# Optimization experiments

Measured on AMD Instinct MI355X. Metric: run time of the kernel, lower is better.

The kernel has to match this reference:

```python
import math
import jax, jax.numpy as jnp
import numpy as np

B, S, D, H = 4, 2048, 1024, 16
HD = D // H
SAMPLING_FACTOR = 5.0


def setup_inputs() -> dict:
    key = jax.random.key(0)
    ks = jax.random.split(key, 6)
    std = 1.0 / math.sqrt(D)
    inp = {
        "x": jax.random.normal(ks[0], (B, S, D), dtype=jnp.float32),
        "Wq": jax.random.normal(ks[1], (D, D), dtype=jnp.float32) * std,
        "bq": jnp.zeros((D,), dtype=jnp.float32),
        "Wk": jax.random.normal(ks[2], (D, D), dtype=jnp.float32) * std,
        "bk": jnp.zeros((D,), dtype=jnp.float32),
        "Wv": jax.random.normal(ks[3], (D, D), dtype=jnp.float32) * std,
        "bv": jnp.zeros((D,), dtype=jnp.float32),
        "Wo": jax.random.normal(ks[4], (D, D), dtype=jnp.float32) * std,
        "bo": jnp.zeros((D,), dtype=jnp.float32),
        "sample_idx": jax.random.randint(ks[5], (S,), 0, S, dtype=jnp.int32),
    }
    return inp


def reference(x, Wq, bq, Wk, bk, Wv, bv, Wo, bo, sample_idx):
    batch, seq_len, d_model = x.shape
    scale = math.sqrt(HD)
    # u = number of top (active) queries; U_part = seq_len here (sampling saturates)
    u = max(1, min(seq_len, int(SAMPLING_FACTOR * math.log(seq_len + 1))))

    def proj(W, b):
        # [B,S,D] -> [B,H,S,hd]
        return (x @ W + b).reshape(batch, seq_len, H, HD).transpose(0, 2, 1, 3)

    Q = proj(Wq, bq)
    K = proj(Wk, bk)
    V = proj(Wv, bv)

    # sparsity measure over sampled keys (with replacement)
    K_sample = K[:, :, sample_idx, :]                     # [B,H,U,hd]
    scores_sample = jnp.einsum("bhsd,bhud->bhsu", Q, K_sample) / scale
    M = scores_sample.max(axis=-1) - scores_sample.mean(axis=-1)  # [B,H,S]

    _, top_idx = jax.lax.top_k(M, u)                      # [B,H,u]

    Q_reduce = jnp.take_along_axis(Q, top_idx[..., None], axis=2)  # [B,H,u,hd]
    attn_scores = jnp.einsum("bhud,bhsd->bhus", Q_reduce, K) / scale
    attn_probs = jax.nn.softmax(attn_scores, axis=-1)
    context = jnp.einsum("bhus,bhsd->bhud", attn_probs, V)        # [B,H,u,hd]

    # fill lazy queries with mean of V, scatter active-query contexts
    V_mean = V.mean(axis=2, keepdims=True)                # [B,H,1,hd]
    out = jnp.broadcast_to(V_mean, (batch, H, seq_len, HD))
    b_idx = jnp.arange(batch)[:, None, None]
    h_idx = jnp.arange(H)[None, :, None]
    out = out.at[b_idx, h_idx, top_idx].set(context)      # [B,H,S,hd]

    out = out.transpose(0, 2, 1, 3).reshape(batch, seq_len, d_model)
    return out @ Wo + bo
```

## Files before the change

### kernel.cpp

```cpp
#include <hip/hip_runtime.h>
#include <math.h>
#include <stdint.h>
#include <stddef.h>

#define BB 4
#define SS 2048
#define DD 1024
#define HH 16
#define HD 64
#define UU 38
#define BH (BB*HH)
#define NROWS (BB*SS)
#define QSZ (BB*HH*SS*HD)
#define NSPLIT 16
#define SPLEN (SS/NSPLIT)
#define QPAD 40

typedef unsigned short ushortT;
typedef unsigned int u32;
typedef __attribute__((ext_vector_type(8))) short bf16x8;
typedef __attribute__((ext_vector_type(4))) float f32x4;

static __device__ __forceinline__ ushortT f2bf(float f) {
  union { float f; unsigned int u; } v; v.f = f;
  unsigned int r = v.u + 0x7fffu + ((v.u >> 16) & 1u);
  return (ushortT)(r >> 16);
}
static __device__ __forceinline__ float bf2f(ushortT h) {
  union { unsigned int u; float f; } v; v.u = ((unsigned int)h) << 16; return v.f;
}
static __device__ __forceinline__ void gld16(const void* g, void* l) {
  __builtin_amdgcn_global_load_lds((const __attribute__((address_space(1))) u32*)g,
                                   (__attribute__((address_space(3))) u32*)l, 16, 0, 0);
}

__global__ __launch_bounds__(256) void split_x(
    const float* __restrict__ x, ushortT* __restrict__ xh, ushortT* __restrict__ xl)
{
  size_t i = ((size_t)blockIdx.x * 256 + threadIdx.x) * 8;
  float4 v0 = *(const float4*)&x[i];
  float4 v1 = *(const float4*)&x[i + 4];
  float fv[8] = {v0.x, v0.y, v0.z, v0.w, v1.x, v1.y, v1.z, v1.w};
  bf16x8 hv, lv;
#pragma unroll
  for (int j = 0; j < 8; ++j) {
    ushortT h = f2bf(fv[j]);
    hv[j] = (short)h;
    lv[j] = (short)f2bf(fv[j] - bf2f(h));
  }
  *(bf16x8*)&xh[i] = hv;
  *(bf16x8*)&xl[i] = lv;
}

__global__ __launch_bounds__(256) void splitT_kernel(
    const float* __restrict__ Wq, const float* __restrict__ Wk, const float* __restrict__ Wv,
    ushortT* __restrict__ WqhT, ushortT* __restrict__ WqlT,
    ushortT* __restrict__ WkhT, ushortT* __restrict__ WklT,
    ushortT* __restrict__ WvhT, ushortT* __restrict__ WvlT)
{
  __shared__ float tile[64][65];
  const int z = blockIdx.z;
  const float* W = (z == 0) ? Wq : (z == 1) ? Wk : Wv;
  ushortT* WhT = (z == 0) ? WqhT : (z == 1) ? WkhT : WvhT;
  ushortT* WlT = (z == 0) ? WqlT : (z == 1) ? WklT : WvlT;
  const int t = threadIdx.x;
  const int bk = blockIdx.y * 64, bn = blockIdx.x * 64;
  const int rr = t >> 4, c4 = (t & 15) * 4;
#pragma unroll
  for (int p = 0; p < 4; ++p) {
    int row = rr + p * 16;
    float4 v = *(const float4*)&W[(size_t)(bk + row) * DD + bn + c4];
    tile[row][c4] = v.x; tile[row][c4+1] = v.y; tile[row][c4+2] = v.z; tile[row][c4+3] = v.w;
  }
  __syncthreads();
  const int n = t & 63, ks = (t >> 6) * 16;
  union { ushortT us[16]; uint4 q[2]; } hb, lb;
#pragma unroll
  for (int j = 0; j < 16; ++j) {
    float f = tile[ks + j][n];
    ushortT h = f2bf(f);
    hb.us[j] = h;
    lb.us[j] = f2bf(f - bf2f(h));
  }
  size_t o = ((size_t)(bn + n) * DD + (size_t)(bk + ks)) >> 3;
  ((uint4*)WhT)[o] = hb.q[0]; ((uint4*)WhT)[o + 1] = hb.q[1];
  ((uint4*)WlT)[o] = lb.q[0]; ((uint4*)WlT)[o + 1] = lb.q[1];
}

__global__ __launch_bounds__(256) void dedupe_kernel(
    const int* __restrict__ sidx, int* __restrict__ uidx, int* __restrict__ ucount,
    float* __restrict__ Vsum, float* __restrict__ Ksum)
{
  __shared__ unsigned bm[64];
  __shared__ int base[64];
  const int t = threadIdx.x;
  for (int i = t; i < BH * HD; i += 256) { Vsum[i] = 0.f; Ksum[i] = 0.f; }
  if (t < 64) bm[t] = 0;
  __syncthreads();
  for (int s = t; s < SS; s += 256) {
    int v = sidx[s];
    atomicOr(&bm[v >> 5], 1u << (v & 31));
  }
  __syncthreads();
  if (t < 64) {
    int c = __popc(bm[t]);
    int pre = c;
#pragma unroll
    for (int off = 1; off < 64; off <<= 1) {
      int o = __shfl_up(pre, off, 64);
      if (t >= off) pre += o;
    }
    base[t] = pre - c;
    if (t == 63) ucount[0] = pre;
  }
  __syncthreads();
  if (t < 64) {
    unsigned m = bm[t];
    int o = base[t];
    while (m) {
      int b = __ffs(m) - 1;
      uidx[o++] = t * 32 + b;
      m &= m - 1;
    }
  }
  __syncthreads();
  int total = ucount[0];
  int padded = (total + 127) & ~127;
  int first = uidx[0];
  for (int i = total + t; i < padded; i += 256) uidx[i] = first;
}

__global__ __launch_bounds__(256, 4) void gemm_qkv(
    const ushortT* __restrict__ Axh, const ushortT* __restrict__ Axl,
    const ushortT* __restrict__ WqhT, const ushortT* __restrict__ WqlT,
    const ushortT* __restrict__ WkhT, const ushortT* __restrict__ WklT,
    const ushortT* __restrict__ WvhT, const ushortT* __restrict__ WvlT,
    const float* __restrict__ bq, const float* __restrict__ bk, const float* __restrict__ bv,
    ushortT* __restrict__ Qhg, ushortT* __restrict__ Qlg,
    ushortT* __restrict__ Khg, ushortT* __restrict__ Klg,
    float* __restrict__ V, float* __restrict__ Vsum)
{
  __shared__ ushortT As[128 * 64];
  __shared__ ushortT Bs[128 * 64];
  const int t = threadIdx.x;
  const int lin = blockIdx.x;
  const int xcd = lin & 7;
  const int idx = lin >> 3;
  const int m_loc = idx & 7;
  const int n_idx = idx >> 3;
  const int m0 = (xcd * 8 + m_loc) * 128;
  const int p = n_idx >> 3;
  const int n0 = (n_idx & 7) * 128;
  const ushortT* Bh = (p == 0) ? WqhT : (p == 1) ? WkhT : WvhT;
  const ushortT* Bl = (p == 0) ? WqlT : (p == 1) ? WklT : WvlT;
  const float* bias = (p == 0) ? bq : (p == 1) ? bk : bv;
  const int NTk = (p == 2) ? 32 : 48;
  const int lane = t & 63, w = t >> 6;
  const int wr = w >> 1, wc = w & 1;
  const int fr = lane & 15, fs = lane >> 4;
  const int srow = t >> 3, sslot = t & 7;
  f32x4 acc[4][4];
#pragma unroll
  for (int i = 0; i < 4; ++i)
#pragma unroll
    for (int j = 0; j < 4; ++j) acc[i][j] = (f32x4){0.f, 0.f, 0.f, 0.f};

  for (int kt = 0; kt < NTk; ++kt) {
    const int seg = kt >> 4;
    const int rk0 = (kt & 15) * 64;
    const ushortT* a_src = (seg == 1) ? Axl : Axh;
    const ushortT* b_src = (seg == 2) ? Bl : Bh;
    __syncthreads();
#pragma unroll
    for (int is = 0; is < 4; ++is) {
      int row = is * 32 + srow;
      int soff = ((sslot ^ (row & 7)) * 8);
      int cb = (is * 256 + (t & 192)) * 8;
      gld16(&a_src[(size_t)(m0 + row) * DD + rk0 + soff], &As[cb]);
      gld16(&b_src[(size_t)(n0 + row) * DD + rk0 + soff], &Bs[cb]);
    }
    __syncthreads();
#pragma unroll
    for (int kk = 0; kk < 2; ++kk) {
      bf16x8 af[4], bf[4];
#pragma unroll
      for (int i = 0; i < 4; ++i) {
        int row = wr * 64 + i * 16 + fr;
        af[i] = *(const bf16x8*)&As[row * 64 + (((kk * 4 + fs) ^ (row & 7)) * 8)];
      }
#pragma unroll
      for (int j = 0; j < 4; ++j) {
        int row = wc * 64 + j * 16 + fr;
        bf[j] = *(const bf16x8*)&Bs[row * 64 + (((kk * 4 + fs) ^ (row & 7)) * 8)];
      }
#pragma unroll
      for (int i = 0; i < 4; ++i)
#pragma unroll
        for (int j = 0; j < 4; ++j)
          acc[i][j] = __builtin_amdgcn_mfma_f32_16x16x32_bf16(af[i], bf[j], acc[i][j], 0, 0, 0);
    }
  }
  float csum[4] = {0.f, 0.f, 0.f, 0.f};
#pragma unroll
  for (int i = 0; i < 4; ++i) {
#pragma unroll
    for (int j = 0; j < 4; ++j) {
      int c = n0 + wc * 64 + j * 16 + fr;
      float bs = bias[c];
      int h = c >> 6, hd = c & 63;
#pragma unroll
      for (int r = 0; r < 4; ++r) {
        int m = m0 + wr * 64 + i * 16 + fs * 4 + r;
        int b = m >> 11, s = m & (SS - 1);
        size_t oidx = (((size_t)(b * HH + h)) * SS + s) * HD + hd;
        float val = acc[i][j][r] + bs;
        if (p == 2) {
          V[oidx] = val;
          csum[j] += val;
        } else {
          ushortT hv = f2bf(val);
          ushortT lv = f2bf(val - bf2f(hv));
          if (p == 0) { Qhg[oidx] = hv; Qlg[oidx] = lv; }
          else        { Khg[oidx] = hv; Klg[oidx] = lv; }
        }
      }
    }
  }
  if (p == 2) {
    __syncthreads();
    float* red = (float*)As;
    int slot = wr * 4 + fs;
#pragma unroll
    for (int j = 0; j < 4; ++j)
      red[(wc * 64 + j * 16 + fr) * 8 + slot] = csum[j];
    __syncthreads();
    if (t < 128) {
      float s = 0.f;
#pragma unroll
      for (int g = 0; g < 8; ++g) s += red[t * 8 + g];
      int c = n0 + t;
      int h = c >> 6, hd = c & 63;
      atomicAdd(&Vsum[((m0 >> 11) * HH + h) * HD + hd], s);
    }
  }
}

__global__ __launch_bounds__(256) void means_kernel(
    const ushortT* __restrict__ Khg, const ushortT* __restrict__ Klg,
    const int* __restrict__ sidx, float* __restrict__ Ksum)
{
  __shared__ float rk[4][64];
  const int bh = blockIdx.x;
  const int sp = blockIdx.y;
  const int t = threadIdx.x;
  const int d = t & 63, pq = t >> 6;
  float ka = 0.f;
  const int r0 = sp * 512 + pq * 128;
  for (int r = r0; r < r0 + 128; ++r) {
    size_t ki = ((size_t)bh * SS + sidx[r]) * HD + d;
    ka += bf2f(Khg[ki]) + bf2f(Klg[ki]);
  }
  rk[pq][d] = ka;
  __syncthreads();
  if (t < 64)
    atomicAdd(&Ksum[bh * HD + t], rk[0][t] + rk[1][t] + rk[2][t] + rk[3][t]);
}

__global__ __launch_bounds__(256, 3) void m_mfma(
    const ushortT* __restrict__ Qhg, const ushortT* __restrict__ Qlg,
    const ushortT* __restrict__ Khg, const ushortT* __restrict__ Klg,
    const int* __restrict__ uidx, const int* __restrict__ ucount,
    const float* __restrict__ Ksum, float* __restrict__ M)
{
  __shared__ ushortT KhL[128 * 64], KlL[128 * 64];
  __shared__ float Mred[2][128];
  __shared__ float km[64];
  const int t = threadIdx.x;
  const int lin = blockIdx.x;
  const int swz = (lin & 7) * 128 + (lin >> 3);
  const int bh = swz >> 4;
  const int s0 = (swz & 15) * 128;
  const int lane = t & 63, w = t >> 6;
  const int wr = w >> 1, wc = w & 1;
  const int fr = lane & 15, fs = lane >> 4;
  if (t < 64) km[t] = Ksum[bh * HD + t] * (1.0f / SS);
  const int srow = t >> 3, sslot = t & 7;
  const int ntiles = (ucount[0] + 127) >> 7;
  const size_t qbase = (size_t)bh * SS + s0;
  float runmax[4][4];
#pragma unroll
  for (int i = 0; i < 4; ++i)
#pragma unroll
    for (int r = 0; r < 4; ++r) runmax[i][r] = -INFINITY;

  for (int ui = 0; ui < ntiles; ++ui) {
    __syncthreads();
#pragma unroll
    for (int is = 0; is < 4; ++is) {
      int row = is * 32 + srow;
      int gr = uidx[ui * 128 + row];
      int soff = ((sslot ^ (row & 7)) * 8);
      int cb = (is * 256 + (t & 192)) * 8;
      size_t ga = ((size_t)bh * SS + gr) * HD + soff;
      gld16(&Khg[ga], &KhL[cb]);
      gld16(&Klg[ga], &KlL[cb]);
    }
    __syncthreads();
    f32x4 acc[4][4];
#pragma unroll
    for (int i = 0; i < 4; ++i)
#pragma unroll
      for (int j = 0; j < 4; ++j) acc[i][j] = (f32x4){0.f, 0.f, 0.f, 0.f};
#pragma unroll
    for (int kk = 0; kk < 2; ++kk) {
      bf16x8 ah[4], al[4], bh[4], bl[4];
#pragma unroll
      for (int i = 0; i < 4; ++i) {
        size_t ga = (qbase + (size_t)(wr * 64 + i * 16 + fr)) * HD + kk * 32 + fs * 8;
        ah[i] = *(const bf16x8*)&Qhg[ga];
        al[i] = *(const bf16x8*)&Qlg[ga];
      }
#pragma unroll
      for (int j = 0; j < 4; ++j) {
        int row = wc * 64 + j * 16 + fr;
        int off = row * 64 + (((kk * 4 + fs) ^ (row & 7)) * 8);
        bh[j] = *(const bf16x8*)&KhL[off];
        bl[j] = *(const bf16x8*)&KlL[off];
      }
#pragma unroll
      for (int i = 0; i < 4; ++i)
#pragma unroll
        for (int j = 0; j < 4; ++j) {
          acc[i][j] = __builtin_amdgcn_mfma_f32_16x16x32_bf16(ah[i], bh[j], acc[i][j], 0, 0, 0);
          acc[i][j] = __builtin_amdgcn_mfma_f32_16x16x32_bf16(ah[i], bl[j], acc[i][j], 0, 0, 0);
          acc[i][j] = __builtin_amdgcn_mfma_f32_16x16x32_bf16(al[i], bh[j], acc[i][j], 0, 0, 0);
        }
    }
#pragma unroll
    for (int i = 0; i < 4; ++i)
#pragma unroll
      for (int j = 0; j < 4; ++j)
#pragma unroll
        for (int r = 0; r < 4; ++r) runmax[i][r] = fmaxf(runmax[i][r], acc[i][j][r]);
  }
#pragma unroll
  for (int i = 0; i < 4; ++i)
#pragma unroll
    for (int r = 0; r < 4; ++r) {
      float v = runmax[i][r];
      v = fmaxf(v, __shfl_xor(v, 1, 64));
      v = fmaxf(v, __shfl_xor(v, 2, 64));
      v = fmaxf(v, __shfl_xor(v, 4, 64));
      v = fmaxf(v, __shfl_xor(v, 8, 64));
      runmax[i][r] = v;
    }
  if (fr == 0) {
#pragma unroll
    for (int i = 0; i < 4; ++i)
#pragma unroll
      for (int r = 0; r < 4; ++r)
        Mred[wc][wr * 64 + i * 16 + fs * 4 + r] = runmax[i][r];
  }
  __syncthreads();
  if (t < 128) {
    float mx = fmaxf(Mred[0][t], Mred[1][t]);
    float md = 0.f;
    const ushortT* qh = &Qhg[(qbase + t) * HD];
    const ushortT* ql = &Qlg[(qbase + t) * HD];
#pragma unroll
    for (int k8 = 0; k8 < 8; ++k8) {
      bf16x8 hv = *(const bf16x8*)&qh[k8 * 8];
      bf16x8 lv = *(const bf16x8*)&ql[k8 * 8];
#pragma unroll
      for (int j = 0; j < 8; ++j)
        md += (bf2f((ushortT)hv[j]) + bf2f((ushortT)lv[j])) * km[k8 * 8 + j];
    }
    M[(size_t)bh * SS + s0 + t] = (mx - md) * 0.125f;
  }
}

__global__ __launch_bounds__(256) void topk_kernel(const float* __restrict__ M,
                                                   int* __restrict__ topi)
{
  __shared__ float rw[4];
  __shared__ int   ri4[4];
  __shared__ int   winner;
  const int t = threadIdx.x, bh = blockIdx.x;
  const int lane = t & 63, w = t >> 6;
  float v[8];
#pragma unroll
  for (int j = 0; j < 8; ++j) v[j] = M[(size_t)bh * SS + t + j * 256];
  for (int it = 0; it < UU; ++it) {
    float bv = v[0]; int bj = 0;
#pragma unroll
    for (int j = 1; j < 8; ++j) if (v[j] > bv) { bv = v[j]; bj = j; }
    int bs = t + bj * 256;
#pragma unroll
    for (int off = 32; off > 0; off >>= 1) {
      float ov = __shfl_xor(bv, off, 64);
      int os = __shfl_xor(bs, off, 64);
      if (ov > bv || (ov == bv && os < bs)) { bv = ov; bs = os; }
    }
    if (lane == 0) { rw[w] = bv; ri4[w] = bs; }
    __syncthreads();
    if (t == 0) {
      float fv = rw[0]; int fsx = ri4[0];
#pragma unroll
      for (int g = 1; g < 4; ++g)
        if (rw[g] > fv || (rw[g] == fv && ri4[g] < fsx)) { fv = rw[g]; fsx = ri4[g]; }
      topi[bh * UU + it] = fsx;
      winner = fsx;
    }
    __syncthreads();
    int wi = winner;
    if ((wi & 255) == t) {
      int jj = wi >> 8;
#pragma unroll
      for (int j = 0; j < 8; ++j) if (j == jj) v[j] = -INFINITY;
    }
  }
}

__global__ __launch_bounds__(256) void attn_flash(
    const ushortT* __restrict__ Qhg, const ushortT* __restrict__ Qlg,
    const ushortT* __restrict__ Khg, const ushortT* __restrict__ Klg,
    const float* __restrict__ V, const int* __restrict__ topi,
    float* __restrict__ pacc, float* __restrict__ pm, float* __restrict__ pl)
{
  __shared__ float Qt[64][68];
  __shared__ float KV[64][68];
  __shared__ float Ps[64][68];
  __shared__ float redA[16][64];
  __shared__ float redB[16][64];
  __shared__ float mrow[64], lrow[64], scl[64];
  const int t  = threadIdx.x;
  const int bh = blockIdx.x;
  const int sp = blockIdx.y;
  const float* Vb = V + (size_t)bh * SS * HD;
  if (t < 64) { mrow[t] = -INFINITY; lrow[t] = 0.f; }
  {
    int q = t >> 2, k4 = (t & 3) * 16;
    float fv[16];
#pragma unroll
    for (int e = 0; e < 16; ++e) fv[e] = 0.f;
    if (q < UU) {
      int qidx = topi[bh * UU + q];
      size_t ga = ((size_t)bh * SS + qidx) * HD + k4;
      bf16x8 h0 = *(const bf16x8*)&Qhg[ga];
      bf16x8 h1 = *(const bf16x8*)&Qhg[ga + 8];
      bf16x8 l0 = *(const bf16x8*)&Qlg[ga];
      bf16x8 l1 = *(const bf16x8*)&Qlg[ga + 8];
#pragma unroll
      for (int j = 0; j < 8; ++j) {
        fv[j]     = bf2f((ushortT)h0[j]) + bf2f((ushortT)l0[j]);
        fv[8 + j] = bf2f((ushortT)h1[j]) + bf2f((ushortT)l1[j]);
      }
    }
#pragma unroll
    for (int e = 0; e < 16; ++e) Qt[k4 + e][q] = fv[e];
  }
  const int q4 = (t & 15) * 4, j4g = (t >> 4) * 4, d4 = (t >> 4) * 4;
  const int lj = t >> 2, lk4 = (t & 3) * 16;
  float acc[4][4] = {};
  for (int s0 = sp * SPLEN; s0 < (sp + 1) * SPLEN; s0 += 64) {
    __syncthreads();
    {
      size_t ga = ((size_t)bh * SS + s0 + lj) * HD + lk4;
      bf16x8 h0 = *(const bf16x8*)&Khg[ga];
      bf16x8 h1 = *(const bf16x8*)&Khg[ga + 8];
      bf16x8 l0 = *(const bf16x8*)&Klg[ga];
      bf16x8 l1 = *(const bf16x8*)&Klg[ga + 8];
#pragma unroll
      for (int j = 0; j < 8; ++j) {
        KV[lk4 + j][lj]     = bf2f((ushortT)h0[j]) + bf2f((ushortT)l0[j]);
        KV[lk4 + 8 + j][lj] = bf2f((ushortT)h1[j]) + bf2f((ushortT)l1[j]);
      }
    }
    __syncthreads();
    float sacc[4][4] = {};
#pragma unroll 16
    for (int k = 0; k < 64; ++k) {
      float4 a = *(const float4*)&Qt[k][q4];
      float4 b = *(const float4*)&KV[k][j4g];
      sacc[0][0] += a.x*b.x; sacc[0][1] += a.x*b.y; sacc[0][2] += a.x*b.z; sacc[0][3] += a.x*b.w;
      sacc[1][0] += a.y*b.x; sacc[1][1] += a.y*b.y; sacc[1][2] += a.y*b.z; sacc[1][3] += a.y*b.w;
      sacc[2][0] += a.z*b.x; sacc[2][1] += a.z*b.y; sacc[2][2] += a.z*b.z; sacc[2][3] += a.z*b.w;
      sacc[3][0] += a.w*b.x; sacc[3][1] += a.w*b.y; sacc[3][2] += a.w*b.z; sacc[3][3] += a.w*b.w;
    }
#pragma unroll
    for (int i = 0; i < 4; ++i) {
      float mx = fmaxf(fmaxf(sacc[i][0], sacc[i][1]), fmaxf(sacc[i][2], sacc[i][3]));
      redA[t >> 4][q4 + i] = mx;
    }
    __syncthreads();
    if (t < 64) {
      float mx = redA[0][t];
#pragma unroll
      for (int g = 1; g < 16; ++g) mx = fmaxf(mx, redA[g][t]);
      float mn = fmaxf(mrow[t], mx * 0.125f);
      scl[t] = __expf(mrow[t] - mn);
      mrow[t] = mn;
    }
    __syncthreads();
    float4 vld[4];
#pragma unroll
    for (int i = 0; i < 4; ++i)
      vld[i] = *(const float4*)&Vb[(size_t)(s0 + lj) * HD + lk4 + 4 * i];
    float psum[4] = {};
#pragma unroll
    for (int i = 0; i < 4; ++i) {
#pragma unroll
      for (int j = 0; j < 4; ++j) {
        float e = __expf(sacc[i][j] * 0.125f - mrow[q4 + i]);
        Ps[j4g + j][q4 + i] = e;
        psum[i] += e;
      }
      redB[t >> 4][q4 + i] = psum[i];
    }
#pragma unroll
    for (int i = 0; i < 4; ++i)
      *(float4*)&KV[lj][lk4 + 4 * i] = vld[i];
    __syncthreads();
    if (t < 64) {
      float ts = redB[0][t];
#pragma unroll
      for (int g = 1; g < 16; ++g) ts += redB[g][t];
      lrow[t] = lrow[t] * scl[t] + ts;
    }
#pragma unroll
    for (int i = 0; i < 4; ++i) {
      float fsc = scl[q4 + i];
      acc[i][0] *= fsc; acc[i][1] *= fsc; acc[i][2] *= fsc; acc[i][3] *= fsc;
    }
#pragma unroll 16
    for (int j = 0; j < 64; ++j) {
      float4 a = *(const float4*)&Ps[j][q4];
      float4 b = *(const float4*)&KV[j][d4];
      acc[0][0] += a.x*b.x; acc[0][1] += a.x*b.y; acc[0][2] += a.x*b.z; acc[0][3] += a.x*b.w;
      acc[1][0] += a.y*b.x; acc[1][1] += a.y*b.y; acc[1][2] += a.y*b.z; acc[1][3] += a.y*b.w;
      acc[2][0] += a.z*b.x; acc[2][1] += a.z*b.y; acc[2][2] += a.z*b.z; acc[2][3] += a.z*b.w;
      acc[3][0] += a.w*b.x; acc[3][1] += a.w*b.y; acc[3][2] += a.w*b.z; acc[3][3] += a.w*b.w;
    }
  }
  const size_t pb = ((size_t)bh * NSPLIT + sp) * QPAD;
#pragma unroll
  for (int i = 0; i < 4; ++i) {
    int q = q4 + i;
    if (q < UU) {
#pragma unroll
      for (int j = 0; j < 4; ++j)
        pacc[(pb + q) * HD + d4 + j] = acc[i][j];
    }
  }
  if (t < UU) { pm[pb + t] = mrow[t]; pl[pb + t] = lrow[t]; }
}

__global__ __launch_bounds__(256) void base_kernel(
    const float* __restrict__ Vsum, const float* __restrict__ Wo,
    const float* __restrict__ bo, float* __restrict__ base)
{
  __shared__ float red[16][BB][16];
  const int t = threadIdx.x;
  const int cl = t & 15, kg = t >> 4;
  const int c = blockIdx.x * 16 + cl;
  float acc[BB] = {};
  for (int k = kg * 64; k < kg * 64 + 64; ++k) {
    float w = Wo[(size_t)k * DD + c];
#pragma unroll
    for (int b = 0; b < BB; ++b) acc[b] += Vsum[b * DD + k] * w;
  }
#pragma unroll
  for (int b = 0; b < BB; ++b) red[kg][b][cl] = acc[b];
  __syncthreads();
  if (t < 64) {
    int b = t >> 4, cc = blockIdx.x * 16 + (t & 15);
    float s = 0.f;
#pragma unroll
    for (int g = 0; g < 16; ++g) s += red[g][b][t & 15];
    base[b * DD + cc] = s * (1.0f / SS) + bo[cc];
  }
}

__global__ void fill_kernel(const float* __restrict__ base, float* __restrict__ out)
{
  size_t i = (size_t)blockIdx.x * 256 + threadIdx.x;
  float4 bv = ((const float4*)base)[(i >> 19) * 256 + (i & 255)];
  ((float4*)out)[i] = bv;
}

__global__ __launch_bounds__(256) void scatter_kernel(
    const float* __restrict__ pacc, const float* __restrict__ pm,
    const float* __restrict__ pl, const float* __restrict__ Vsum,
    const int* __restrict__ topi, const float* __restrict__ Wo,
    float* __restrict__ out)
{
  __shared__ float delta[64];
  const int t  = threadIdx.x;
  const int bh = blockIdx.x;
  const int u  = blockIdx.y;
  const int b = bh >> 4, h = bh & 15;
  const int s = topi[bh * UU + u];
  if (t < 64) {
    float mv[NSPLIT];
    float ms = -INFINITY;
#pragma unroll
    for (int sp = 0; sp < NSPLIT; ++sp) {
      mv[sp] = pm[((size_t)bh * NSPLIT + sp) * QPAD + u];
      ms = fmaxf(ms, mv[sp]);
    }
    float l = 0.f, c = 0.f;
#pragma unroll
    for (int sp = 0; sp < NSPLIT; ++sp) {
      float wv = __expf(mv[sp] - ms);
      l += wv * pl[((size_t)bh * NSPLIT + sp) * QPAD + u];
      c += wv * pacc[(((size_t)bh * NSPLIT + sp) * QPAD + u) * HD + t];
    }
    delta[t] = c / l - Vsum[bh * HD + t] * (1.0f / SS);
  }
  __syncthreads();
  float* orow = out + ((size_t)b * SS + s) * DD;
#pragma unroll
  for (int j = 0; j < 4; ++j) {
    int c = t + j * 256;
    float acc = 0.f;
#pragma unroll 8
    for (int d = 0; d < 64; ++d) acc += delta[d] * Wo[(size_t)(h * HD + d) * DD + c];
    atomicAdd(&orow[c], acc);
  }
}

extern "C" void kernel_launch(void* const* d_in, const int* in_sizes, int n_in,
                              void* d_out, int out_size, void* d_ws, size_t ws_size,
                              hipStream_t stream) {
  const float* x  = (const float*)d_in[0];
  const float* Wq = (const float*)d_in[1];
  const float* bq = (const float*)d_in[2];
  const float* Wk = (const float*)d_in[3];
  const float* bk = (const float*)d_in[4];
  const float* Wv = (const float*)d_in[5];
  const float* bv = (const float*)d_in[6];
  const float* Wo = (const float*)d_in[7];
  const float* bo = (const float*)d_in[8];
  const int* sidx = (const int*)d_in[9];
  float* out = (float*)d_out;

  float* f     = (float*)d_ws;
  float* V     = f;
  float* Ksum  = f + (size_t)QSZ;
  float* Vsum  = Ksum + BH * HD;
  float* Mbuf  = Vsum + BH * HD;
  float* base  = Mbuf + (size_t)BH * SS;
  float* ctx   = base + BB * DD;
  float* pacc  = ctx + (size_t)BH * UU * HD;
  float* pm    = pacc + (size_t)BH * NSPLIT * QPAD * HD;
  float* pl    = pm + (size_t)BH * NSPLIT * QPAD;
  int*   topi  = (int*)(pl + (size_t)BH * NSPLIT * QPAD);
  int*   uidx  = topi + 4096;
  int*   ucount= uidx + 4096;
  ushortT* usp = (ushortT*)(ucount + 64);
  ushortT* WqhT = usp;
  ushortT* WqlT = WqhT + (size_t)DD * DD;
  ushortT* WkhT = WqlT + (size_t)DD * DD;
  ushortT* WklT = WkhT + (size_t)DD * DD;
  ushortT* WvhT = WklT + (size_t)DD * DD;
  ushortT* WvlT = WvhT + (size_t)DD * DD;
  ushortT* xh   = WvlT + (size_t)DD * DD;
  ushortT* xl   = xh + (size_t)NROWS * DD;
  ushortT* Qhg  = xl + (size_t)NROWS * DD;
  ushortT* Qlg  = Qhg + (size_t)QSZ;
  ushortT* Khg  = Qlg + (size_t)QSZ;
  ushortT* Klg  = Khg + (size_t)QSZ;

  split_x<<<NROWS * DD / (256 * 8), 256, 0, stream>>>(x, xh, xl);
  splitT_kernel<<<dim3(16, 16, 3), 256, 0, stream>>>(Wq, Wk, Wv, WqhT, WqlT,
                                                     WkhT, WklT, WvhT, WvlT);
  dedupe_kernel<<<1, 256, 0, stream>>>(sidx, uidx, ucount, Vsum, Ksum);
  gemm_qkv<<<1536, 256, 0, stream>>>(xh, xl, WqhT, WqlT, WkhT, WklT, WvhT, WvlT,
                                     bq, bk, bv, Qhg, Qlg, Khg, Klg, V, Vsum);
  means_kernel<<<dim3(BH, 4), 256, 0, stream>>>(Khg, Klg, sidx, Ksum);
  m_mfma<<<1024, 256, 0, stream>>>(Qhg, Qlg, Khg, Klg, uidx, ucount, Ksum, Mbuf);
  topk_kernel<<<BH, 256, 0, stream>>>(Mbuf, topi);
  attn_flash<<<dim3(BH, NSPLIT), 256, 0, stream>>>(Qhg, Qlg, Khg, Klg, V, topi, pacc, pm, pl);
  base_kernel<<<DD / 16, 256, 0, stream>>>(Vsum, Wo, bo, base);
  fill_kernel<<<(NROWS * DD / 4) / 256, 256, 0, stream>>>(base, out);
  scatter_kernel<<<dim3(BH, UU), 256, 0, stream>>>(pacc, pm, pl, Vsum, topi, Wo, out);
}
```

Measured before the change: 388.3 us.

## Pipeline QKV GEMM with 4-stage LDS ring and larger 256x128 tiles

Rewrites the split-bf16 QKV projection GEMM to use 512-thread blocks on 256x128 output tiles, with a four-slot LDS ring buffer of 32-wide K slices. Loads are issued three stages ahead, using explicit vmcnt waits and raw barriers in place of the double __syncthreads per K tile, and MFMA sections are raised with s_setprio. The aim is to hide global-load latency behind MFMA work and cut synchronization stalls. In exchange it uses 96 KB of LDS per block, which lowers occupancy, and the hand-tuned waitcnt accounting is fragile.

```diff
diff --git a/kernel.cpp b/kernel.cpp
--- a/kernel.cpp
+++ b/kernel.cpp
@@ -130,7 +130,7 @@
   for (int i = total + t; i < padded; i += 256) uidx[i] = first;
 }
 
-__global__ __launch_bounds__(256, 4) void gemm_qkv(
+__global__ __launch_bounds__(512) void gemm_qkv(
     const ushortT* __restrict__ Axh, const ushortT* __restrict__ Axl,
     const ushortT* __restrict__ WqhT, const ushortT* __restrict__ WqlT,
     const ushortT* __restrict__ WkhT, const ushortT* __restrict__ WklT,
@@ -140,77 +140,109 @@
     ushortT* __restrict__ Khg, ushortT* __restrict__ Klg,
     float* __restrict__ V, float* __restrict__ Vsum)
 {
-  __shared__ ushortT As[128 * 64];
-  __shared__ ushortT Bs[128 * 64];
+  __shared__ ushortT L[49152];
   const int t = threadIdx.x;
   const int lin = blockIdx.x;
   const int xcd = lin & 7;
   const int idx = lin >> 3;
-  const int m_loc = idx & 7;
-  const int n_idx = idx >> 3;
-  const int m0 = (xcd * 8 + m_loc) * 128;
+  const int m0 = (xcd * 4 + (idx & 3)) * 256;
+  const int n_idx = idx >> 2;
   const int p = n_idx >> 3;
   const int n0 = (n_idx & 7) * 128;
   const ushortT* Bh = (p == 0) ? WqhT : (p == 1) ? WkhT : WvhT;
   const ushortT* Bl = (p == 0) ? WqlT : (p == 1) ? WklT : WvlT;
   const float* bias = (p == 0) ? bq : (p == 1) ? bk : bv;
   const int NTk = (p == 2) ? 32 : 48;
-  const int lane = t & 63, w = t >> 6;
-  const int wr = w >> 1, wc = w & 1;
+  const int NPH = NTk * 2;
+  const int lane = t & 63, wid = t >> 6;
+  const int wrm = wid >> 1, wcn = wid & 1;
   const int fr = lane & 15, fs = lane >> 4;
-  const int srow = t >> 3, sslot = t & 7;
+  const int wub = (t & ~63) * 8;
+
   f32x4 acc[4][4];
 #pragma unroll
   for (int i = 0; i < 4; ++i)
 #pragma unroll
     for (int j = 0; j < 4; ++j) acc[i][j] = (f32x4){0.f, 0.f, 0.f, 0.f};
 
-  for (int kt = 0; kt < NTk; ++kt) {
-    const int seg = kt >> 4;
-    const int rk0 = (kt & 15) * 64;
+  auto stage_pair = [&](int P) {
+    const int TP = P >> 1, kk = P & 1;
+    const int seg = TP >> 4;
+    const int rk0 = (TP & 15) * 64 + kk * 32;
     const ushortT* a_src = (seg == 1) ? Axl : Axh;
     const ushortT* b_src = (seg == 2) ? Bl : Bh;
-    __syncthreads();
-#pragma unroll
-    for (int is = 0; is < 4; ++is) {
-      int row = is * 32 + srow;
-      int soff = ((sslot ^ (row & 7)) * 8);
-      int cb = (is * 256 + (t & 192)) * 8;
-      gld16(&a_src[(size_t)(m0 + row) * DD + rk0 + soff], &As[cb]);
-      gld16(&b_src[(size_t)(n0 + row) * DD + rk0 + soff], &Bs[cb]);
-    }
-    __syncthreads();
-#pragma unroll
-    for (int kk = 0; kk < 2; ++kk) {
-      bf16x8 af[4], bf[4];
-#pragma unroll
-      for (int i = 0; i < 4; ++i) {
-        int row = wr * 64 + i * 16 + fr;
-        af[i] = *(const bf16x8*)&As[row * 64 + (((kk * 4 + fs) ^ (row & 7)) * 8)];
-      }
-#pragma unroll
-      for (int j = 0; j < 4; ++j) {
-        int row = wc * 64 + j * 16 + fr;
-        bf[j] = *(const bf16x8*)&Bs[row * 64 + (((kk * 4 + fs) ^ (row & 7)) * 8)];
-      }
-#pragma unroll
-      for (int i = 0; i < 4; ++i)
-#pragma unroll
-        for (int j = 0; j < 4; ++j)
-          acc[i][j] = __builtin_amdgcn_mfma_f32_16x16x32_bf16(af[i], bf[j], acc[i][j], 0, 0, 0);
-    }
-  }
+    const int aslot = (P & 3) * 8192;
+    const int bslot = 32768 + (P & 3) * 4096;
+#pragma unroll
+    for (int l = 0; l < 2; ++l) {
+      int lu = l * 4096 + t * 8;
+      int row = lu >> 5;
+      int chunk = (lu >> 3) & 3;
+      int sch = chunk ^ ((row >> 2) & 3);
+      gld16(&a_src[(size_t)(m0 + row) * DD + rk0 + sch * 8],
+            &L[aslot + l * 4096 + wub]);
+    }
+    {
+      int row = t >> 2;
+      int chunk = t & 3;
+      int sch = chunk ^ ((row >> 2) & 3);
+      gld16(&b_src[(size_t)(n0 + row) * DD + rk0 + sch * 8],
+            &L[bslot + wub]);
+    }
+  };
+  auto compute = [&](int g) {
+    const int aslot = (g & 3) * 8192;
+    const int bslot = 32768 + (g & 3) * 4096;
+    bf16x8 a[4], b[4];
+#pragma unroll
+    for (int i = 0; i < 4; ++i) {
+      int row = wrm * 64 + i * 16 + fr;
+      a[i] = *(const bf16x8*)&L[aslot + row * 32 + ((fs ^ ((row >> 2) & 3)) * 8)];
+    }
+#pragma unroll
+    for (int j = 0; j < 4; ++j) {
+      int row = wcn * 64 + j * 16 + fr;
+      b[j] = *(const bf16x8*)&L[bslot + row * 32 + ((fs ^ ((row >> 2) & 3)) * 8)];
+    }
+    __builtin_amdgcn_s_setprio(1);
+#pragma unroll
+    for (int i = 0; i < 4; ++i)
+#pragma unroll
+      for (int j = 0; j < 4; ++j)
+        acc[i][j] = __builtin_amdgcn_mfma_f32_16x16x32_bf16(a[i], b[j], acc[i][j], 0, 0, 0);
+    __builtin_amdgcn_s_setprio(0);
+  };
+
+  stage_pair(0); stage_pair(1); stage_pair(2);
+  asm volatile("s_waitcnt vmcnt(6)" ::: "memory");
+  __builtin_amdgcn_s_barrier();
+
+  for (int g = 0; g < NPH; ++g) {
+    if (g + 3 < NPH) stage_pair(g + 3);
+    compute(g);
+    if (g < NPH - 3) {
+      asm volatile("s_waitcnt vmcnt(6)" ::: "memory");
+      __builtin_amdgcn_s_barrier();
+    } else if (g == NPH - 3) {
+      asm volatile("s_waitcnt vmcnt(3)" ::: "memory");
+      __builtin_amdgcn_s_barrier();
+    } else if (g == NPH - 2) {
+      asm volatile("s_waitcnt vmcnt(0)" ::: "memory");
+      __builtin_amdgcn_s_barrier();
+    }
+  }
+
   float csum[4] = {0.f, 0.f, 0.f, 0.f};
 #pragma unroll
   for (int i = 0; i < 4; ++i) {
 #pragma unroll
     for (int j = 0; j < 4; ++j) {
-      int c = n0 + wc * 64 + j * 16 + fr;
+      int c = n0 + wcn * 64 + j * 16 + fr;
       float bs = bias[c];
       int h = c >> 6, hd = c & 63;
 #pragma unroll
       for (int r = 0; r < 4; ++r) {
-        int m = m0 + wr * 64 + i * 16 + fs * 4 + r;
+        int m = m0 + wrm * 64 + i * 16 + fs * 4 + r;
         int b = m >> 11, s = m & (SS - 1);
         size_t oidx = (((size_t)(b * HH + h)) * SS + s) * HD + hd;
         float val = acc[i][j][r] + bs;
@@ -227,17 +259,17 @@
     }
   }
   if (p == 2) {
-    __syncthreads();
-    float* red = (float*)As;
-    int slot = wr * 4 + fs;
+    __builtin_amdgcn_s_barrier();
+    float* red = (float*)L;
+    int slot = wrm * 4 + fs;
 #pragma unroll
     for (int j = 0; j < 4; ++j)
-      red[(wc * 64 + j * 16 + fr) * 8 + slot] = csum[j];
+      red[(wcn * 64 + j * 16 + fr) * 16 + slot] = csum[j];
     __syncthreads();
     if (t < 128) {
       float s = 0.f;
 #pragma unroll
-      for (int g = 0; g < 8; ++g) s += red[t * 8 + g];
+      for (int g = 0; g < 16; ++g) s += red[t * 16 + g];
       int c = n0 + t;
       int h = c >> 6, hd = c & 63;
       atomicAdd(&Vsum[((m0 >> 11) * HH + h) * HD + hd], s);
@@ -675,8 +707,8 @@
   splitT_kernel<<<dim3(16, 16, 3), 256, 0, stream>>>(Wq, Wk, Wv, WqhT, WqlT,
                                                      WkhT, WklT, WvhT, WvlT);
   dedupe_kernel<<<1, 256, 0, stream>>>(sidx, uidx, ucount, Vsum, Ksum);
-  gemm_qkv<<<1536, 256, 0, stream>>>(xh, xl, WqhT, WqlT, WkhT, WklT, WvhT, WvlT,
-                                     bq, bk, bv, Qhg, Qlg, Khg, Klg, V, Vsum);
+  gemm_qkv<<<768, 512, 0, stream>>>(xh, xl, WqhT, WqlT, WkhT, WklT, WvhT, WvlT,
+                                    bq, bk, bv, Qhg, Qlg, Khg, Klg, V, Vsum);
   means_kernel<<<dim3(BH, 4), 256, 0, stream>>>(Khg, Klg, sidx, Ksum);
   m_mfma<<<1024, 256, 0, stream>>>(Qhg, Qlg, Khg, Klg, uidx, ucount, Ksum, Mbuf);
   topk_kernel<<<BH, 256, 0, stream>>>(Mbuf, topi);
```

Result: slower. 424.6 us (+9.3%).
